# Kernel optimization log

Measured on AMD Instinct MI355X. Metric: run time of the kernel, lower is better.

The kernel has to match this reference:

```python
import jax, jax.numpy as jnp
import numpy as np

N = 262144  # points
C = 256     # backbone_out_channels
K = 20      # semantic_num_classes
BN_EPS = 1e-3
EPS = 1e-8
IGNORE = -1


def setup_inputs() -> dict:
    key = jax.random.key(0)
    ks = jax.random.split(key, 12)
    feat = jax.random.normal(ks[0], (N, C), dtype=jnp.float32)
    coord = jax.random.normal(ks[1], (N, 3), dtype=jnp.float32)
    instance_centroid = jax.random.normal(ks[2], (N, 3), dtype=jnp.float32)
    segment = jax.random.randint(ks[3], (N,), 0, K, dtype=jnp.int32)
    instance = jax.random.randint(ks[4], (N,), 0, 1000, dtype=jnp.int32)
    # bias_head: Linear(C,C) -> BN1d(C) -> ReLU -> Linear(C,3)
    w1 = jax.random.normal(ks[5], (C, C), dtype=jnp.float32) * 0.02
    b1 = jnp.zeros((C,), dtype=jnp.float32)
    gamma = jnp.ones((C,), dtype=jnp.float32)
    beta = jnp.zeros((C,), dtype=jnp.float32)
    w2 = jax.random.normal(ks[6], (C, 3), dtype=jnp.float32) * 0.02
    b2 = jnp.zeros((3,), dtype=jnp.float32)
    # seg_head: Linear(C, K)
    ws = jax.random.normal(ks[7], (C, K), dtype=jnp.float32) * 0.02
    bs = jnp.zeros((K,), dtype=jnp.float32)
    return dict(feat=feat, coord=coord, instance_centroid=instance_centroid,
                segment=segment, instance=instance,
                w1=w1, b1=b1, gamma=gamma, beta=beta, w2=w2, b2=b2, ws=ws, bs=bs)


def reference(feat, coord, instance_centroid, segment, instance,
              w1, b1, gamma, beta, w2, b2, ws, bs):
    # bias head: Linear -> BatchNorm1d (training stats) -> ReLU -> Linear
    h = feat @ w1 + b1                                  # [N, C]
    mu = jnp.mean(h, axis=0)
    var = jnp.mean((h - mu) ** 2, axis=0)               # biased var (torch BN)
    h = (h - mu) * jax.lax.rsqrt(var + BN_EPS) * gamma + beta
    h = jax.nn.relu(h)
    bias_pred = h @ w2 + b2                             # [N, 3]

    logit_pred = feat @ ws + bs                         # [N, K]

    # semantic cross-entropy with ignore_index
    valid = segment != IGNORE
    tgt = jnp.where(valid, segment, 0)
    logp = jax.nn.log_softmax(logit_pred, axis=-1)
    nll = -jnp.take_along_axis(logp, tgt[:, None], axis=1)[:, 0]
    vf = valid.astype(logit_pred.dtype)
    seg_loss = jnp.sum(nll * vf) / (jnp.sum(vf) + EPS)

    # masked bias L1 loss
    mask = (instance != IGNORE).astype(bias_pred.dtype)
    bias_gt = instance_centroid - coord                 # [N, 3]
    bias_dist = jnp.sum(jnp.abs(bias_pred - bias_gt), axis=-1)
    msum = jnp.sum(mask) + EPS
    bias_l1_loss = jnp.sum(bias_dist * mask) / msum

    # masked cosine (direction) loss
    pred_n = bias_pred / (jnp.linalg.norm(bias_pred, axis=1, keepdims=True) + EPS)
    gt_n = bias_gt / (jnp.linalg.norm(bias_gt, axis=1, keepdims=True) + EPS)
    cos = -jnp.sum(pred_n * gt_n, axis=-1)
    bias_cosine_loss = jnp.sum(cos * mask) / msum

    loss = seg_loss + bias_l1_loss + bias_cosine_loss
    return jnp.stack([loss, seg_loss, bias_l1_loss, bias_cosine_loss])
```

## Files before the change

### kernel.cpp

```cpp
#include <hip/hip_runtime.h>
#include <cstdio>
#include <cstdint>

typedef unsigned int u32;
typedef unsigned short u16;
typedef short bf16x8 __attribute__((ext_vector_type(8)));
typedef float f32x4 __attribute__((ext_vector_type(4)));

#define NPTS 262144
#define CDIM 256
#define KCLS 20
#define NBLK 4096
#define NSLOT 256
#define LSLOT 256

#define OFF_WT    ((size_t)134217728)
#define OFF_W2T   (OFF_WT + (size_t)163840)
#define OFF_AGGBN (OFF_W2T + (size_t)8192)
#define OFF_AGGNL (OFF_AGGBN + (size_t)524288)
#define OFF_AGGL  (OFF_AGGNL + (size_t)2048)
#define OFF_AB    (OFF_AGGL + (size_t)4096)
#define WS_NEED   (OFF_AB + (size_t)2048)
#define MEMSET_OFF OFF_AGGBN
#define MEMSET_LEN ((size_t)(524288 + 2048 + 4096))

__device__ __forceinline__ u16 bf16rne(float x) {
    u32 u = __float_as_uint(x);
    u32 r = u + 0x7FFFu + ((u >> 16) & 1u);
    return (u16)(r >> 16);
}
__device__ __forceinline__ float bf2f(u16 b) {
    return __uint_as_float(((u32)b) << 16);
}

__global__ void k_prep(const float* __restrict__ w1, const float* __restrict__ wsm,
                       const float* __restrict__ w2,
                       u16* __restrict__ Wt2, u16* __restrict__ w2t) {
    int k = blockIdx.x;
    int n = threadIdx.x;
    float v = 0.f;
    if (n < 256) v = w1[k * 256 + n];
    else if (n < 256 + KCLS) v = wsm[k * KCLS + (n - 256)];
    Wt2[((size_t)(k >> 3) * 320 + n) * 8 + (k & 7)] = bf16rne(v);
    if (n < 16) w2t[n * 256 + k] = bf16rne((n < 3) ? w2[k * 3 + n] : 0.f);
}

__global__ __launch_bounds__(256) void k_gemm(
    const float* __restrict__ feat, const float* __restrict__ b1,
    const float* __restrict__ bs, const int* __restrict__ segment,
    const u16* __restrict__ Wt2, u16* __restrict__ h_out,
    float* __restrict__ aggBN, float* __restrict__ aggNLL)
{
    __shared__ uint4 smem4[2560];
    uint4* const As4 = smem4;
    uint4* const Bs4 = smem4 + 512;

    const int t = threadIdx.x;
    const int lane = t & 63;
    const int wv = t >> 6;
    const int q = lane >> 4;
    const int i16 = lane & 15;
    const int row0 = blockIdx.x * 64;
    const int slot = blockIdx.x & (NSLOT - 1);

    const f32x4 fz = {0.f, 0.f, 0.f, 0.f};
    f32x4 acc[4][4];
    f32x4 lacc[2];
#pragma unroll
    for (int r = 0; r < 4; ++r)
#pragma unroll
        for (int c = 0; c < 4; ++c) acc[r][c] = fz;
    lacc[0] = fz; lacc[1] = fz;

    const int sm = t >> 2;
    const int sq = t & 3;
    const float* fsrc = feat + (size_t)(row0 + sm) * 256 + sq * 8;
    const int wsl = sm ^ (sq << 2);
    const int As_slot0 = sq * 64 + wsl;
    const int As_slot1 = (sq + 4) * 64 + wsl;

    float4 f0 = *(const float4*)(fsrc);
    float4 f1 = *(const float4*)(fsrc + 4);
    float4 f2 = *(const float4*)(fsrc + 32);
    float4 f3 = *(const float4*)(fsrc + 36);

#pragma unroll 1
    for (int kc = 0; kc < 4; ++kc) {
        {
            uint4 pk;
            pk.x = (u32)bf16rne(f0.x) | ((u32)bf16rne(f0.y) << 16);
            pk.y = (u32)bf16rne(f0.z) | ((u32)bf16rne(f0.w) << 16);
            pk.z = (u32)bf16rne(f1.x) | ((u32)bf16rne(f1.y) << 16);
            pk.w = (u32)bf16rne(f1.z) | ((u32)bf16rne(f1.w) << 16);
            As4[As_slot0] = pk;
            pk.x = (u32)bf16rne(f2.x) | ((u32)bf16rne(f2.y) << 16);
            pk.y = (u32)bf16rne(f2.z) | ((u32)bf16rne(f2.w) << 16);
            pk.z = (u32)bf16rne(f3.x) | ((u32)bf16rne(f3.y) << 16);
            pk.w = (u32)bf16rne(f3.z) | ((u32)bf16rne(f3.w) << 16);
            As4[As_slot1] = pk;
        }
#pragma unroll
        for (int i = 0; i < 4; ++i) {
            const u16* src0 = Wt2 + ((size_t)(kc * 8 + wv) * 320 + i * 64 + lane) * 8;
            u32* dst0 = (u32*)&Bs4[wv * 256 + i * 64];
            __builtin_amdgcn_global_load_lds(
                (const __attribute__((address_space(1))) u32*)src0,
                (__attribute__((address_space(3))) u32*)dst0, 16, 0, 0);
            const u16* src1 = Wt2 + ((size_t)(kc * 8 + wv + 4) * 320 + i * 64 + lane) * 8;
            u32* dst1 = (u32*)&Bs4[(wv + 4) * 256 + i * 64];
            __builtin_amdgcn_global_load_lds(
                (const __attribute__((address_space(1))) u32*)(src1),
                (__attribute__((address_space(3))) u32*)dst1, 16, 0, 0);
        }
        __syncthreads();

        float4 fn0, fn1, fn2, fn3;
        if (kc < 3) {
            const float* p = fsrc + (kc + 1) * 64;
            fn0 = *(const float4*)(p);
            fn1 = *(const float4*)(p + 4);
            fn2 = *(const float4*)(p + 32);
            fn3 = *(const float4*)(p + 36);
        }

#pragma unroll
        for (int s = 0; s < 2; ++s) {
            const int kq = s * 4 + q;
            bf16x8 lbf[2];
#pragma unroll
            for (int x = 0; x < 2; ++x)
                lbf[x] = *(const bf16x8*)(Wt2 +
                    ((size_t)(kc * 8 + kq) * 320 + 256 + x * 16 + i16) * 8);
            bf16x8 bfr[4], af[4], la;
#pragma unroll
            for (int c = 0; c < 4; ++c)
                bfr[c] = *(const bf16x8*)&Bs4[kq * 256 + wv * 64 + c * 16 + i16];
#pragma unroll
            for (int r = 0; r < 4; ++r)
                af[r] = *(const bf16x8*)&As4[kq * 64 + ((r * 16 + i16) ^ (q << 2))];
            la = *(const bf16x8*)&As4[kq * 64 + ((wv * 16 + i16) ^ (q << 2))];

#pragma unroll
            for (int r = 0; r < 4; ++r)
#pragma unroll
                for (int c = 0; c < 4; ++c)
                    acc[r][c] = __builtin_amdgcn_mfma_f32_16x16x32_bf16(af[r], bfr[c], acc[r][c], 0, 0, 0);
#pragma unroll
            for (int x = 0; x < 2; ++x)
                lacc[x] = __builtin_amdgcn_mfma_f32_16x16x32_bf16(la, lbf[x], lacc[x], 0, 0, 0);
        }
        __syncthreads();
        f0 = fn0; f1 = fn1; f2 = fn2; f3 = fn3;
    }

    float b1v[4];
#pragma unroll
    for (int c = 0; c < 4; ++c) b1v[c] = b1[wv * 64 + c * 16 + i16];
    float bsv0 = bs[i16];
    float bsv1 = (16 + i16 < KCLS) ? bs[16 + i16] : 0.f;

    float nllacc = 0.f, cntacc = 0.f;
#pragma unroll
    for (int j = 0; j < 4; ++j) {
        int rowr = row0 + wv * 16 + q * 4 + j;
        float l0 = lacc[0][j] + bsv0;
        float l1raw = lacc[1][j] + bsv1;
        float l1m = (i16 < 4) ? l1raw : -3.0e38f;
        float mx = fmaxf(l0, l1m);
#pragma unroll
        for (int d = 1; d < 16; d <<= 1) mx = fmaxf(mx, __shfl_xor(mx, d));
        float s = __expf(l0 - mx) + ((i16 < 4) ? __expf(l1raw - mx) : 0.f);
#pragma unroll
        for (int d = 1; d < 16; d <<= 1) s += __shfl_xor(s, d);
        int tg = segment[rowr];
        float v0 = __shfl(l0, (lane & 48) + (tg & 15));
        float v1 = __shfl(l1raw, (lane & 48) + ((tg - 16) & 15));
        float lt = (tg < 16) ? v0 : v1;
        if (i16 == 0 && tg >= 0) {
            nllacc += __logf(s) + mx - lt;
            cntacc += 1.f;
        }
    }
#pragma unroll
    for (int d = 1; d < 64; d <<= 1) {
        nllacc += __shfl_xor(nllacc, d);
        cntacc += __shfl_xor(cntacc, d);
    }
    if (lane == 0) {
        atomicAdd(aggNLL + slot * 2 + 0, nllacc);
        atomicAdd(aggNLL + slot * 2 + 1, cntacc);
    }

#pragma unroll
    for (int c = 0; c < 4; ++c) {
        float s1 = 0.f, s2 = 0.f;
#pragma unroll
        for (int r = 0; r < 4; ++r)
#pragma unroll
            for (int j = 0; j < 4; ++j) {
                float v = acc[r][c][j] + b1v[c];
                s1 += v; s2 = fmaf(v, v, s2);
            }
        s1 += __shfl_xor(s1, 16); s1 += __shfl_xor(s1, 32);
        s2 += __shfl_xor(s2, 16); s2 += __shfl_xor(s2, 32);
        if (q == 0) {
            int ch = wv * 64 + c * 16 + i16;
            atomicAdd(aggBN + slot * 512 + ch, s1);
            atomicAdd(aggBN + slot * 512 + 256 + ch, s2);
        }
    }

    u16* Ht = (u16*)smem4;
#pragma unroll
    for (int r = 0; r < 4; ++r)
#pragma unroll
        for (int c = 0; c < 4; ++c)
#pragma unroll
            for (int j = 0; j < 4; ++j) {
                float v = acc[r][c][j] + b1v[c];
                int rw = r * 16 + q * 4 + j;
                int cl = wv * 64 + c * 16 + i16;
                Ht[rw * 264 + cl] = bf16rne(v);
            }
    __syncthreads();
#pragma unroll
    for (int i = 0; i < 8; ++i) {
        int chunk = i * 256 + t;
        int m = chunk >> 5;
        int off = (chunk & 31) * 16;
        uint4 v = *(const uint4*)((const char*)smem4 + m * 528 + off);
        *(uint4*)((char*)h_out + (size_t)(row0 + m) * 512 + off) = v;
    }
}

__global__ void k_reduce(const float* __restrict__ gamma, const float* __restrict__ beta,
                         const float* __restrict__ aggBN,
                         float* __restrict__ Aarr, float* __restrict__ Barr) {
    int c = blockIdx.x;
    int l = threadIdx.x;
    float s1 = 0.f, s2 = 0.f;
#pragma unroll
    for (int i = 0; i < 4; ++i) {
        int s = l + i * 64;
        s1 += aggBN[s * 512 + c];
        s2 += aggBN[s * 512 + 256 + c];
    }
#pragma unroll
    for (int d = 1; d < 64; d <<= 1) {
        s1 += __shfl_xor(s1, d);
        s2 += __shfl_xor(s2, d);
    }
    if (l == 0) {
        const float inv = 1.f / (float)NPTS;
        float mu = s1 * inv;
        float var = fmaxf(s2 * inv - mu * mu, 0.f);
        float a = gamma[c] * rsqrtf(var + 1e-3f);
        Aarr[c] = a;
        Barr[c] = beta[c] - mu * a;
    }
}

__global__ __launch_bounds__(256, 4) void k_loss(
    const u16* __restrict__ h, const float* __restrict__ Aarr, const float* __restrict__ Barr,
    const u16* __restrict__ w2t, const float* __restrict__ b2,
    const float* __restrict__ coord, const float* __restrict__ cent,
    const int* __restrict__ inst, float* __restrict__ aggL)
{
    __shared__ u16 hs[64 * 264];
    __shared__ float As_l[256], Bs_l[256];
    __shared__ float bp[4][16][4];
    __shared__ float red[12];

    const int t = threadIdx.x;
    const int lane = t & 63;
    const int wv = t >> 6;
    const int q = lane >> 4;
    const int i16 = lane & 15;
    const int row0 = blockIdx.x * 64;

#pragma unroll
    for (int i = 0; i < 8; ++i) {
        int chunk = i * 256 + t;
        int m = chunk >> 5;
        int off = (chunk & 31) * 16;
        *(uint4*)((char*)hs + m * 528 + off) =
            *(const uint4*)((const char*)h + (size_t)(row0 + m) * 512 + off);
    }
    if (t < 256) { As_l[t] = Aarr[t]; Bs_l[t] = Barr[t]; }

    bf16x8 wfr[8];
#pragma unroll
    for (int kc = 0; kc < 8; ++kc)
        wfr[kc] = *(const bf16x8*)(w2t + (size_t)i16 * 256 + kc * 32 + q * 8);
    float b2x = b2[0], b2y = b2[1], b2z = b2[2];
    __syncthreads();

    const f32x4 fz = {0.f, 0.f, 0.f, 0.f};
    f32x4 c = fz;
#pragma unroll
    for (int kc = 0; kc < 8; ++kc) {
        bf16x8 hf = *(const bf16x8*)(hs + (wv * 16 + i16) * 264 + kc * 32 + q * 8);
        float4 a0 = *(const float4*)(As_l + kc * 32 + q * 8);
        float4 a1 = *(const float4*)(As_l + kc * 32 + q * 8 + 4);
        float4 b0 = *(const float4*)(Bs_l + kc * 32 + q * 8);
        float4 b1 = *(const float4*)(Bs_l + kc * 32 + q * 8 + 4);
        float av[8] = {a0.x, a0.y, a0.z, a0.w, a1.x, a1.y, a1.z, a1.w};
        float bv[8] = {b0.x, b0.y, b0.z, b0.w, b1.x, b1.y, b1.z, b1.w};
        bf16x8 hn;
#pragma unroll
        for (int j = 0; j < 8; ++j) {
            float x = fmaxf(fmaf(bf2f(((const u16*)&hf)[j]), av[j], bv[j]), 0.f);
            ((u16*)&hn)[j] = bf16rne(x);
        }
        c = __builtin_amdgcn_mfma_f32_16x16x32_bf16(hn, wfr[kc], c, 0, 0, 0);
    }

    if (i16 < 3) {
#pragma unroll
        for (int j = 0; j < 4; ++j) bp[wv][q * 4 + j][i16] = c[j];
    }
    float l1a = 0.f, cosa = 0.f, ma = 0.f;
    if (lane < 16) {
        int row = row0 + wv * 16 + lane;
        float4 P = *(const float4*)bp[wv][lane];
        float bpx = P.x + b2x, bpy = P.y + b2y, bpz = P.z + b2z;
        const float* cp = coord + (size_t)row * 3;
        const float* ip = cent + (size_t)row * 3;
        float gx = ip[0] - cp[0], gy = ip[1] - cp[1], gz = ip[2] - cp[2];
        float mk = (inst[row] != -1) ? 1.f : 0.f;
        float l1 = fabsf(bpx - gx) + fabsf(bpy - gy) + fabsf(bpz - gz);
        float np = sqrtf(fmaf(bpx, bpx, fmaf(bpy, bpy, bpz * bpz)));
        float ng = sqrtf(fmaf(gx, gx, fmaf(gy, gy, gz * gz)));
        float dp = fmaf(bpx, gx, fmaf(bpy, gy, bpz * gz));
        float cosv = -dp / ((np + 1e-8f) * (ng + 1e-8f));
        l1a = l1 * mk;
        cosa = cosv * mk;
        ma = mk;
    }
#pragma unroll
    for (int d = 1; d < 64; d <<= 1) {
        l1a += __shfl_xor(l1a, d);
        cosa += __shfl_xor(cosa, d);
        ma += __shfl_xor(ma, d);
    }
    if (lane == 0) { red[wv] = l1a; red[4 + wv] = cosa; red[8 + wv] = ma; }
    __syncthreads();
    if (t == 0) {
        int slot = blockIdx.x & (LSLOT - 1);
        atomicAdd(aggL + slot * 4 + 0, red[0] + red[1] + red[2] + red[3]);
        atomicAdd(aggL + slot * 4 + 1, red[4] + red[5] + red[6] + red[7]);
        atomicAdd(aggL + slot * 4 + 2, red[8] + red[9] + red[10] + red[11]);
    }
}

__global__ void k_final(const float* __restrict__ aggNLL, const float* __restrict__ aggL,
                        float* __restrict__ out) {
    int lane = threadIdx.x;
    float nll = 0.f, cnt = 0.f, l1 = 0.f, cs = 0.f, mk = 0.f;
#pragma unroll
    for (int i = 0; i < 4; ++i) {
        int s = lane + i * 64;
        nll += aggNLL[s * 2 + 0];
        cnt += aggNLL[s * 2 + 1];
        l1 += aggL[s * 4 + 0];
        cs += aggL[s * 4 + 1];
        mk += aggL[s * 4 + 2];
    }
#pragma unroll
    for (int d = 1; d < 64; d <<= 1) {
        nll += __shfl_xor(nll, d);
        cnt += __shfl_xor(cnt, d);
        l1 += __shfl_xor(l1, d);
        cs += __shfl_xor(cs, d);
        mk += __shfl_xor(mk, d);
    }
    if (lane == 0) {
        float seg = nll / (cnt + 1e-8f);
        float l1l = l1 / (mk + 1e-8f);
        float csl = cs / (mk + 1e-8f);
        out[0] = seg + l1l + csl;
        out[1] = seg;
        out[2] = l1l;
        out[3] = csl;
    }
}

extern "C" void kernel_launch(void* const* d_in, const int* in_sizes, int n_in,
                              void* d_out, int out_size, void* d_ws, size_t ws_size,
                              hipStream_t stream) {
    const float* feat   = (const float*)d_in[0];
    const float* coord  = (const float*)d_in[1];
    const float* cent   = (const float*)d_in[2];
    const int* segment  = (const int*)d_in[3];
    const int* inst     = (const int*)d_in[4];
    const float* w1     = (const float*)d_in[5];
    const float* b1     = (const float*)d_in[6];
    const float* gamma  = (const float*)d_in[7];
    const float* beta   = (const float*)d_in[8];
    const float* w2     = (const float*)d_in[9];
    const float* b2     = (const float*)d_in[10];
    const float* wsm    = (const float*)d_in[11];
    const float* bs     = (const float*)d_in[12];
    float* out = (float*)d_out;

    char* wsb = (char*)d_ws;
    u16* h_ws    = (u16*)wsb;
    u16* Wt2     = (u16*)(wsb + OFF_WT);
    u16* w2t     = (u16*)(wsb + OFF_W2T);
    float* aggBN = (float*)(wsb + OFF_AGGBN);
    float* aggNL = (float*)(wsb + OFF_AGGNL);
    float* aggL  = (float*)(wsb + OFF_AGGL);
    float* Aarr  = (float*)(wsb + OFF_AB);
    float* Barr  = Aarr + 256;

    if (ws_size < WS_NEED)
        fprintf(stderr, "kernel_launch: ws_size=%zu < needed %zu — WILL CORRUPT\n",
                ws_size, (size_t)WS_NEED);

    hipMemsetAsync(wsb + MEMSET_OFF, 0, MEMSET_LEN, stream);
    k_prep<<<256, 320, 0, stream>>>(w1, wsm, w2, Wt2, w2t);
    k_gemm<<<NBLK, 256, 0, stream>>>(feat, b1, bs, segment, Wt2, h_ws, aggBN, aggNL);
    k_reduce<<<256, 64, 0, stream>>>(gamma, beta, aggBN, Aarr, Barr);
    k_loss<<<4096, 256, 0, stream>>>(h_ws, Aarr, Barr, w2t, b2, coord, cent, inst, aggL);
    k_final<<<1, 64, 0, stream>>>(aggNL, aggL, out);
}
```

Baseline: 479.1 us.

## Store H in MFMA fragment order so loss kernel loads directly to registers

```diff
diff --git a/kernel.cpp b/kernel.cpp
--- a/kernel.cpp
+++ b/kernel.cpp
@@ -225,11 +225,13 @@
     __syncthreads();
 #pragma unroll
     for (int i = 0; i < 8; ++i) {
-        int chunk = i * 256 + t;
-        int m = chunk >> 5;
-        int off = (chunk & 31) * 16;
-        uint4 v = *(const uint4*)((const char*)smem4 + m * 528 + off);
-        *(uint4*)((char*)h_out + (size_t)(row0 + m) * 512 + off) = v;
+        int c2 = i * 256 + t;
+        int rb = c2 >> 9;
+        int kc = (c2 >> 6) & 7;
+        int qq = (c2 >> 4) & 3;
+        int r16 = c2 & 15;
+        uint4 v = *(const uint4*)((const char*)smem4 + (rb * 16 + r16) * 528 + kc * 64 + qq * 16);
+        *(uint4*)((char*)h_out + (size_t)(blockIdx.x * 4 + rb) * 8192 + (size_t)(c2 & 511) * 16) = v;
     }
 }
 
@@ -260,16 +262,13 @@
     }
 }
 
-__global__ __launch_bounds__(256, 4) void k_loss(
+__global__ __launch_bounds__(256) void k_loss(
     const u16* __restrict__ h, const float* __restrict__ Aarr, const float* __restrict__ Barr,
     const u16* __restrict__ w2t, const float* __restrict__ b2,
     const float* __restrict__ coord, const float* __restrict__ cent,
     const int* __restrict__ inst, float* __restrict__ aggL)
 {
-    __shared__ u16 hs[64 * 264];
-    __shared__ float As_l[256], Bs_l[256];
     __shared__ float bp[4][16][4];
-    __shared__ float red[12];
 
     const int t = threadIdx.x;
     const int lane = t & 63;
@@ -277,39 +276,34 @@
     const int q = lane >> 4;
     const int i16 = lane & 15;
     const int row0 = blockIdx.x * 64;
-
-#pragma unroll
-    for (int i = 0; i < 8; ++i) {
-        int chunk = i * 256 + t;
-        int m = chunk >> 5;
-        int off = (chunk & 31) * 16;
-        *(uint4*)((char*)hs + m * 528 + off) =
-            *(const uint4*)((const char*)h + (size_t)(row0 + m) * 512 + off);
-    }
-    if (t < 256) { As_l[t] = Aarr[t]; Bs_l[t] = Barr[t]; }
+    const int rb = blockIdx.x * 4 + wv;
+
+    const u16* hb = h + (size_t)rb * 4096 + q * 128 + i16 * 8;
+    bf16x8 hf[8];
+#pragma unroll
+    for (int kc = 0; kc < 8; ++kc)
+        hf[kc] = *(const bf16x8*)(hb + kc * 512);
 
     bf16x8 wfr[8];
 #pragma unroll
     for (int kc = 0; kc < 8; ++kc)
         wfr[kc] = *(const bf16x8*)(w2t + (size_t)i16 * 256 + kc * 32 + q * 8);
     float b2x = b2[0], b2y = b2[1], b2z = b2[2];
-    __syncthreads();
 
     const f32x4 fz = {0.f, 0.f, 0.f, 0.f};
     f32x4 c = fz;
 #pragma unroll
     for (int kc = 0; kc < 8; ++kc) {
-        bf16x8 hf = *(const bf16x8*)(hs + (wv * 16 + i16) * 264 + kc * 32 + q * 8);
-        float4 a0 = *(const float4*)(As_l + kc * 32 + q * 8);
-        float4 a1 = *(const float4*)(As_l + kc * 32 + q * 8 + 4);
-        float4 b0 = *(const float4*)(Bs_l + kc * 32 + q * 8);
-        float4 b1 = *(const float4*)(Bs_l + kc * 32 + q * 8 + 4);
+        float4 a0 = *(const float4*)(Aarr + kc * 32 + q * 8);
+        float4 a1 = *(const float4*)(Aarr + kc * 32 + q * 8 + 4);
+        float4 b0 = *(const float4*)(Barr + kc * 32 + q * 8);
+        float4 b1 = *(const float4*)(Barr + kc * 32 + q * 8 + 4);
         float av[8] = {a0.x, a0.y, a0.z, a0.w, a1.x, a1.y, a1.z, a1.w};
         float bv[8] = {b0.x, b0.y, b0.z, b0.w, b1.x, b1.y, b1.z, b1.w};
         bf16x8 hn;
 #pragma unroll
         for (int j = 0; j < 8; ++j) {
-            float x = fmaxf(fmaf(bf2f(((const u16*)&hf)[j]), av[j], bv[j]), 0.f);
+            float x = fmaxf(fmaf(bf2f(((const u16*)&hf[kc])[j]), av[j], bv[j]), 0.f);
             ((u16*)&hn)[j] = bf16rne(x);
         }
         c = __builtin_amdgcn_mfma_f32_16x16x32_bf16(hn, wfr[kc], c, 0, 0, 0);
@@ -343,13 +337,11 @@
         cosa += __shfl_xor(cosa, d);
         ma += __shfl_xor(ma, d);
     }
-    if (lane == 0) { red[wv] = l1a; red[4 + wv] = cosa; red[8 + wv] = ma; }
-    __syncthreads();
-    if (t == 0) {
+    if (lane == 0) {
         int slot = blockIdx.x & (LSLOT - 1);
-        atomicAdd(aggL + slot * 4 + 0, red[0] + red[1] + red[2] + red[3]);
-        atomicAdd(aggL + slot * 4 + 1, red[4] + red[5] + red[6] + red[7]);
-        atomicAdd(aggL + slot * 4 + 2, red[8] + red[9] + red[10] + red[11]);
+        atomicAdd(aggL + slot * 4 + 0, l1a);
+        atomicAdd(aggL + slot * 4 + 1, cosa);
+        atomicAdd(aggL + slot * 4 + 2, ma);
     }
 }
 
```

Result: no change. 484.2 us (+1.0%).
